# Kernel tuning notes

Measured on AMD Instinct MI355X. Metric: run time of the kernel, lower is better.

## Reference

```python
import jax, jax.numpy as jnp
import numpy as np

MAX_EDGE_LENGTH = 100.0  # filtration cap from cfg['self_supervised']['max_edge_length']


def pairwise_dist(x):
    # Euclidean pairwise distances, [N, N]
    sq = jnp.sum(x * x, axis=-1)
    d2 = sq[:, None] + sq[None, :] - 2.0 * (x @ x.T)
    return jnp.sqrt(jnp.maximum(d2, 0.0) + 1e-12)


def mst_edge_weights(D):
    """Prim's MST over dense distance matrix D [N,N]. Returns N-1 edge weights.
    These weights are exactly the H0 death times of the Vietoris-Rips filtration
    (all H0 features are born at 0)."""
    N = D.shape[0]
    dist0 = D[0]                                   # min distance from tree to each node
    in_tree0 = jnp.zeros((N,), bool).at[0].set(True)

    def step(carry, _):
        dist, in_tree = carry
        masked = jnp.where(in_tree, jnp.inf, dist)
        j = jnp.argmin(masked)
        w = masked[j]                              # weight of edge added to MST
        in_tree = in_tree.at[j].set(True)
        dist = jnp.minimum(dist, D[j])
        return (dist, in_tree), w

    _, weights = jax.lax.scan(step, (dist0, in_tree0), None, length=N - 1)
    return weights


def h0_deaths(x):
    # H0 persistence diagram deaths (births are all 0), capped at max_edge_length
    return jnp.minimum(mst_edge_weights(pairwise_dist(x)), MAX_EDGE_LENGTH)


def setup_inputs() -> dict:
    key = jax.random.key(0)
    k1, k2 = jax.random.split(key)
    N, Dm = 4096, 128
    x_1 = jax.random.normal(k1, (N, Dm), dtype=jnp.float32)
    # correlated second view, as in a siamese/self-supervised setting
    x_2 = x_1 + 0.1 * jax.random.normal(k2, (N, Dm), dtype=jnp.float32)
    return {"x_1": x_1, "x_2": x_2, "plot": 0}


def reference(x_1, x_2, plot):
    # MSE representation loss
    representation_loss = jnp.mean((x_1 - x_2) ** 2)
    # H0 persistence diagrams via Vietoris-Rips (MST formulation)
    d1 = jnp.sort(h0_deaths(x_1))
    d2 = jnp.sort(h0_deaths(x_2))
    # Wasserstein-1 distance between the two H0 diagrams (births all 0,
    # equal cardinality => optimal matching is the sorted matching of deaths)
    topological_loss = jnp.sum(jnp.abs(d1 - d2))
    return representation_loss + topological_loss
```

## Files before the change

### kernel.cpp

```cpp
#include <hip/hip_runtime.h>
#include <hip/hip_fp16.h>

#define NPT 4096
#define DM 128
#define ROUNDS 12
#define INF64 0xFFFFFFFFFFFFFFFFull

typedef _Float16 f16x8 __attribute__((ext_vector_type(8)));
typedef _Float16 f16x2 __attribute__((ext_vector_type(2)));
typedef float f32x4 __attribute__((ext_vector_type(4)));

__global__ __launch_bounds__(256) void init_kernel(unsigned* __restrict__ comp,
                                                   unsigned long long* __restrict__ compbest,
                                                   float* __restrict__ w,
                                                   unsigned* __restrict__ cnt,
                                                   float* __restrict__ rep) {
    int i = blockIdx.x * blockDim.x + threadIdx.x;
    comp[i] = (unsigned)(i & (NPT - 1));
    compbest[i] = INF64;
    w[i] = 0.0f;
    if (i < 2) cnt[i] = 0u;
    if (i == 0) rep[0] = 0.0f;
}

__global__ __launch_bounds__(256) void prep_kernel(const float* __restrict__ x1,
                                                   const float* __restrict__ x2,
                                                   _Float16* __restrict__ Xh,
                                                   float* __restrict__ norms) {
    const int wv = threadIdx.x >> 6, ln = threadIdx.x & 63;
    const int row = blockIdx.x * 4 + wv;
    const float* src = (row < NPT) ? (x1 + (size_t)row * DM)
                                   : (x2 + (size_t)(row - NPT) * DM);
    float2 v = *(const float2*)(src + ln * 2);
    _Float16 h0 = (_Float16)v.x, h1 = (_Float16)v.y;
    f16x2 p; p[0] = h0; p[1] = h1;
    *(f16x2*)(Xh + (size_t)row * DM + ln * 2) = p;
    float a = (float)h0, b = (float)h1;
    float s = a * a + b * b;
    #pragma unroll
    for (int off = 32; off > 0; off >>= 1) s += __shfl_down(s, off);
    if (ln == 0) norms[row] = s;
}

__global__ __launch_bounds__(256) void gram_kernel(const _Float16* __restrict__ Xh,
                                                   const float* __restrict__ norms,
                                                   __half* __restrict__ Dall) {
    const int mat = blockIdx.y;
    const _Float16* __restrict__ X = Xh + (size_t)mat * NPT * DM;
    const float* __restrict__ nrm = norms + mat * NPT;
    __half* __restrict__ D = Dall + (size_t)mat * NPT * NPT;

    int idx = blockIdx.x;
    int J = (int)((sqrtf(8.0f * (float)idx + 1.0f) - 1.0f) * 0.5f);
    while ((J + 1) * (J + 2) / 2 <= idx) ++J;
    while (J * (J + 1) / 2 > idx) --J;
    const int I = idx - J * (J + 1) / 2;

    const int t = threadIdx.x;
    const int wv = t >> 6, ln = t & 63;
    const int rowBase = I * 128 + (wv >> 1) * 64;
    const int colBase = J * 128 + (wv & 1) * 64;
    const int lr = ln & 15;
    const int kg = ln >> 4;

    f32x4 acc[4][4];
    #pragma unroll
    for (int m = 0; m < 4; ++m)
        #pragma unroll
        for (int n = 0; n < 4; ++n)
            acc[m][n] = (f32x4){0.f, 0.f, 0.f, 0.f};

    #pragma unroll
    for (int ks = 0; ks < 4; ++ks) {
        const int k0 = ks * 32 + kg * 8;
        f16x8 a[4], b[4];
        #pragma unroll
        for (int m = 0; m < 4; ++m)
            a[m] = *(const f16x8*)(X + (size_t)(rowBase + m * 16 + lr) * DM + k0);
        #pragma unroll
        for (int n = 0; n < 4; ++n)
            b[n] = *(const f16x8*)(X + (size_t)(colBase + n * 16 + lr) * DM + k0);
        #pragma unroll
        for (int m = 0; m < 4; ++m)
            #pragma unroll
            for (int n = 0; n < 4; ++n)
                acc[m][n] = __builtin_amdgcn_mfma_f32_16x16x32_f16(a[m], b[n], acc[m][n], 0, 0, 0);
    }

    float nr[16], nc[4];
    #pragma unroll
    for (int m = 0; m < 4; ++m)
        #pragma unroll
        for (int q = 0; q < 4; ++q)
            nr[m * 4 + q] = nrm[rowBase + m * 16 + kg * 4 + q];
    #pragma unroll
    for (int n = 0; n < 4; ++n) nc[n] = nrm[colBase + n * 16 + lr];

    #pragma unroll
    for (int m = 0; m < 4; ++m) {
        #pragma unroll
        for (int n = 0; n < 4; ++n) {
            #pragma unroll
            for (int q = 0; q < 4; ++q) {
                const int r = rowBase + m * 16 + kg * 4 + q;
                const int c = colBase + n * 16 + lr;
                float d2 = nr[m * 4 + q] + nc[n] - 2.0f * acc[m][n][q];
                float d = sqrtf(fmaxf(d2, 0.0f) + 1e-12f);
                __half hd = __float2half(d);
                D[(size_t)r * NPT + c] = hd;
                if (I != J) D[(size_t)c * NPT + r] = hd;
            }
        }
    }
}

__global__ __launch_bounds__(1024) void boruvka_a(const __half* __restrict__ Dall,
                                                  const unsigned* __restrict__ compAll,
                                                  unsigned long long* __restrict__ compbestAll,
                                                  const unsigned* __restrict__ cnt) {
    const int mat = blockIdx.y;
    if (cnt[mat] >= NPT - 1u) return;
    const __half* __restrict__ D = Dall + (size_t)mat * NPT * NPT;
    const unsigned* __restrict__ comp = compAll + mat * NPT;
    unsigned long long* __restrict__ compbest = compbestAll + mat * NPT;

    __shared__ unsigned short lcomp[NPT];
    const int t = threadIdx.x;
    for (int i = t; i < NPT; i += 1024) lcomp[i] = (unsigned short)comp[i];
    __syncthreads();

    const int wv = t >> 6, ln = t & 63;
    const int node = blockIdx.x * 16 + wv;
    const unsigned ci = lcomp[node];
    const unsigned* __restrict__ row = (const unsigned*)(D + (size_t)node * NPT);

    unsigned best = 0xFFFFFFFFu;
    #pragma unroll
    for (int k = 0; k < 8; ++k) {
        const int jb = k * 512 + ln * 8;
        uint4 dv = *(const uint4*)(row + (jb >> 1));
        uint4 cv = *(const uint4*)&lcomp[jb];
        const unsigned dp[4] = {dv.x, dv.y, dv.z, dv.w};
        const unsigned cp[4] = {cv.x, cv.y, cv.z, cv.w};
        #pragma unroll
        for (int q = 0; q < 4; ++q) {
            int j0 = jb + q * 2;
            unsigned k0 = (dp[q] << 16) | (unsigned)j0;
            unsigned k1 = (dp[q] & 0xFFFF0000u) | (unsigned)(j0 + 1);
            if ((cp[q] & 0xFFFFu) == ci) k0 = 0xFFFFFFFFu;
            if ((cp[q] >> 16) == ci)     k1 = 0xFFFFFFFFu;
            unsigned m = k0 < k1 ? k0 : k1;
            best = best < m ? best : m;
        }
    }
    #pragma unroll
    for (int off = 32; off > 0; off >>= 1) {
        unsigned o = __shfl_down(best, off);
        best = best < o ? best : o;
    }
    if (ln == 0 && best != 0xFFFFFFFFu) {
        unsigned h = best >> 16;
        unsigned j = best & 0xFFFFu;
        unsigned mn = (unsigned)node < j ? (unsigned)node : j;
        unsigned mx = (unsigned)node < j ? j : (unsigned)node;
        unsigned long long key64 = ((unsigned long long)h << 48) |
                                   ((unsigned long long)mn << 32) |
                                   ((unsigned long long)mx << 16) |
                                   (unsigned long long)j;
        atomicMin(&compbest[ci], key64);
    }
}

__global__ __launch_bounds__(1024) void boruvka_cd(unsigned* __restrict__ compAll,
                                                   unsigned long long* __restrict__ compbestAll,
                                                   float* __restrict__ wAll,
                                                   unsigned* __restrict__ cntAll) {
    const int mat = blockIdx.x;
    if (cntAll[mat] >= NPT - 1u) return;
    unsigned* __restrict__ comp = compAll + mat * NPT;
    unsigned long long* __restrict__ compbest = compbestAll + mat * NPT;
    float* __restrict__ w = wAll + mat * NPT;
    unsigned* __restrict__ cnt = cntAll + mat;

    __shared__ unsigned short par[NPT];
    const int t = threadIdx.x;

    for (int c = t; c < NPT; c += 1024) {
        unsigned p = (unsigned)c;
        unsigned long long key = compbest[c];
        if (comp[c] == (unsigned)c && key != INF64) {
            unsigned jout = (unsigned)(key & 0xFFFFull);
            unsigned c2 = comp[jout];
            unsigned long long k2 = compbest[c2];
            bool mutual = (k2 >> 16) == (key >> 16);
            if (!mutual || (unsigned)c < c2) {
                unsigned short hb = (unsigned short)(key >> 48);
                float wv = fminf(__half2float(__ushort_as_half(hb)), 100.0f);
                unsigned slot = atomicAdd(cnt, 1u);
                w[slot] = wv;
            }
            p = (mutual && (unsigned)c < c2) ? (unsigned)c : c2;
        }
        par[c] = (unsigned short)p;
    }
    __syncthreads();

    for (int it = 0; it < 12; ++it) {
        unsigned short np[4];
        #pragma unroll
        for (int q = 0; q < 4; ++q) np[q] = par[par[t + q * 1024]];
        __syncthreads();
        #pragma unroll
        for (int q = 0; q < 4; ++q) par[t + q * 1024] = np[q];
        __syncthreads();
    }

    for (int c = t; c < NPT; c += 1024) {
        comp[c] = par[comp[c]];
        compbest[c] = INF64;
    }
}

__global__ __launch_bounds__(256) void rep_kernel(const float4* __restrict__ x1,
                                                  const float4* __restrict__ x2,
                                                  float* __restrict__ acc) {
    int idx = blockIdx.x * blockDim.x + threadIdx.x;
    int stride = gridDim.x * blockDim.x;
    float s = 0.f;
    for (int i = idx; i < NPT * DM / 4; i += stride) {
        float4 a = x1[i], b = x2[i];
        float d0 = a.x - b.x, d1 = a.y - b.y, d2 = a.z - b.z, d3 = a.w - b.w;
        s += d0 * d0 + d1 * d1 + d2 * d2 + d3 * d3;
    }
    #pragma unroll
    for (int off = 32; off > 0; off >>= 1) s += __shfl_down(s, off);
    __shared__ float partial[4];
    int wv = threadIdx.x >> 6, ln = threadIdx.x & 63;
    if (ln == 0) partial[wv] = s;
    __syncthreads();
    if (threadIdx.x == 0) {
        float tot = partial[0] + partial[1] + partial[2] + partial[3];
        atomicAdd(acc, tot);
    }
}

__global__ __launch_bounds__(1024) void sort_kernel(float* __restrict__ wAll) {
    float* __restrict__ w = wAll + blockIdx.x * NPT;
    __shared__ float s[NPT];
    const int t = threadIdx.x;
    for (int i = t; i < NPT; i += 1024) s[i] = w[i];
    __syncthreads();

    for (int k = 2; k <= NPT; k <<= 1) {
        for (int j = k >> 1; j > 0; j >>= 1) {
            for (int i = t; i < NPT; i += 1024) {
                int ixj = i ^ j;
                if (ixj > i) {
                    bool up = (i & k) == 0;
                    float a = s[i], b = s[ixj];
                    if ((a > b) == up) { s[i] = b; s[ixj] = a; }
                }
            }
            __syncthreads();
        }
    }
    for (int i = t; i < NPT; i += 1024) w[i] = s[i];
}

__global__ __launch_bounds__(1024) void final2_kernel(const float* __restrict__ w,
                                                      const float* __restrict__ rep,
                                                      float* __restrict__ out) {
    const int t = threadIdx.x;
    float loc = 0.f;
    for (int i = t; i < NPT; i += 1024) loc += fabsf(w[i] - w[NPT + i]);
    #pragma unroll
    for (int off = 32; off > 0; off >>= 1) loc += __shfl_down(loc, off);
    __shared__ float reds[16];
    int wv = t >> 6, ln = t & 63;
    if (ln == 0) reds[wv] = loc;
    __syncthreads();
    if (t == 0) {
        float tot = 0.f;
        #pragma unroll
        for (int i = 0; i < 16; ++i) tot += reds[i];
        out[0] = tot + rep[0] * (1.0f / (NPT * DM));
    }
}

extern "C" void kernel_launch(void* const* d_in, const int* in_sizes, int n_in,
                              void* d_out, int out_size, void* d_ws, size_t ws_size,
                              hipStream_t stream) {
    const float* x1 = (const float*)d_in[0];
    const float* x2 = (const float*)d_in[1];
    float* out = (float*)d_out;

    char* ws = (char*)d_ws;
    __half* D = (__half*)ws;
    size_t off = (size_t)2 * NPT * NPT * sizeof(__half);
    _Float16* Xh = (_Float16*)(ws + off);
    off += (size_t)2 * NPT * DM * sizeof(_Float16);
    float* norms = (float*)(ws + off);
    off += (size_t)2 * NPT * sizeof(float);
    unsigned long long* compbest = (unsigned long long*)(ws + off);
    off += (size_t)2 * NPT * sizeof(unsigned long long);
    float* w = (float*)(ws + off);
    off += (size_t)2 * NPT * sizeof(float);
    unsigned* comp = (unsigned*)(ws + off);
    off += (size_t)2 * NPT * sizeof(unsigned);
    unsigned* cnt = (unsigned*)(ws + off);
    off += 4 * sizeof(unsigned);
    float* rep = (float*)(ws + off);

    init_kernel<<<2 * NPT / 256, 256, 0, stream>>>(comp, compbest, w, cnt, rep);

    prep_kernel<<<2 * NPT / 4, 256, 0, stream>>>(x1, x2, Xh, norms);

    gram_kernel<<<dim3(528, 2), 256, 0, stream>>>(Xh, norms, D);

    for (int r = 0; r < ROUNDS; ++r) {
        boruvka_a<<<dim3(NPT / 16, 2), 1024, 0, stream>>>(D, comp, compbest, cnt);
        boruvka_cd<<<2, 1024, 0, stream>>>(comp, compbest, w, cnt);
    }

    rep_kernel<<<256, 256, 0, stream>>>((const float4*)x1, (const float4*)x2, rep);

    sort_kernel<<<2, 1024, 0, stream>>>(w);

    final2_kernel<<<1, 1024, 0, stream>>>(w, rep, out);
}
```

Before: 341.4 us.

## Fuse Boruvka rounds, sort, and reductions into one cooperative persistent kernel

Replaces the 24 per-round Boruvka kernel launches plus the rep, sort and final kernels with a single cooperative kernel of 256 blocks that uses grid.sync between phases. Rounds exit early once both MSTs are complete. The repr-loss reduction now runs on idle blocks alongside the sort. The gram kernel also drops the symmetric triangular tiling and computes the full square grid, doubling its tiles in exchange for contiguous single writes and no index decoding. The cost is grid-wide barriers and only 256 blocks doing the row-min scans.

```diff
diff --git a/kernel.cpp b/kernel.cpp
--- a/kernel.cpp
+++ b/kernel.cpp
@@ -1,5 +1,8 @@
 #include <hip/hip_runtime.h>
 #include <hip/hip_fp16.h>
+#include <hip/hip_cooperative_groups.h>
+
+namespace cg = cooperative_groups;
 
 #define NPT 4096
 #define DM 128
@@ -50,11 +53,8 @@
     const float* __restrict__ nrm = norms + mat * NPT;
     __half* __restrict__ D = Dall + (size_t)mat * NPT * NPT;
 
-    int idx = blockIdx.x;
-    int J = (int)((sqrtf(8.0f * (float)idx + 1.0f) - 1.0f) * 0.5f);
-    while ((J + 1) * (J + 2) / 2 <= idx) ++J;
-    while (J * (J + 1) / 2 > idx) --J;
-    const int I = idx - J * (J + 1) / 2;
+    const int I = blockIdx.x >> 5;
+    const int J = blockIdx.x & 31;
 
     const int t = threadIdx.x;
     const int wv = t >> 6, ln = t & 63;
@@ -106,184 +106,186 @@
                 const int c = colBase + n * 16 + lr;
                 float d2 = nr[m * 4 + q] + nc[n] - 2.0f * acc[m][n][q];
                 float d = sqrtf(fmaxf(d2, 0.0f) + 1e-12f);
-                __half hd = __float2half(d);
-                D[(size_t)r * NPT + c] = hd;
-                if (I != J) D[(size_t)c * NPT + r] = hd;
-            }
-        }
-    }
-}
-
-__global__ __launch_bounds__(1024) void boruvka_a(const __half* __restrict__ Dall,
-                                                  const unsigned* __restrict__ compAll,
-                                                  unsigned long long* __restrict__ compbestAll,
-                                                  const unsigned* __restrict__ cnt) {
-    const int mat = blockIdx.y;
-    if (cnt[mat] >= NPT - 1u) return;
+                D[(size_t)r * NPT + c] = __float2half(d);
+            }
+        }
+    }
+}
+
+__global__ __launch_bounds__(1024) void mst_coop(const __half* __restrict__ Dall,
+                                                 unsigned* __restrict__ compAll,
+                                                 unsigned long long* __restrict__ compbestAll,
+                                                 float* __restrict__ wAll,
+                                                 unsigned* __restrict__ cntAll,
+                                                 const float4* __restrict__ x1,
+                                                 const float4* __restrict__ x2,
+                                                 float* __restrict__ rep,
+                                                 float* __restrict__ out) {
+    cg::grid_group grid = cg::this_grid();
+    const int bid = blockIdx.x;
+    const int mat = bid >> 7;
+    const int mb = bid & 127;
     const __half* __restrict__ D = Dall + (size_t)mat * NPT * NPT;
-    const unsigned* __restrict__ comp = compAll + mat * NPT;
-    unsigned long long* __restrict__ compbest = compbestAll + mat * NPT;
-
-    __shared__ unsigned short lcomp[NPT];
-    const int t = threadIdx.x;
-    for (int i = t; i < NPT; i += 1024) lcomp[i] = (unsigned short)comp[i];
-    __syncthreads();
-
-    const int wv = t >> 6, ln = t & 63;
-    const int node = blockIdx.x * 16 + wv;
-    const unsigned ci = lcomp[node];
-    const unsigned* __restrict__ row = (const unsigned*)(D + (size_t)node * NPT);
-
-    unsigned best = 0xFFFFFFFFu;
-    #pragma unroll
-    for (int k = 0; k < 8; ++k) {
-        const int jb = k * 512 + ln * 8;
-        uint4 dv = *(const uint4*)(row + (jb >> 1));
-        uint4 cv = *(const uint4*)&lcomp[jb];
-        const unsigned dp[4] = {dv.x, dv.y, dv.z, dv.w};
-        const unsigned cp[4] = {cv.x, cv.y, cv.z, cv.w};
-        #pragma unroll
-        for (int q = 0; q < 4; ++q) {
-            int j0 = jb + q * 2;
-            unsigned k0 = (dp[q] << 16) | (unsigned)j0;
-            unsigned k1 = (dp[q] & 0xFFFF0000u) | (unsigned)(j0 + 1);
-            if ((cp[q] & 0xFFFFu) == ci) k0 = 0xFFFFFFFFu;
-            if ((cp[q] >> 16) == ci)     k1 = 0xFFFFFFFFu;
-            unsigned m = k0 < k1 ? k0 : k1;
-            best = best < m ? best : m;
-        }
-    }
-    #pragma unroll
-    for (int off = 32; off > 0; off >>= 1) {
-        unsigned o = __shfl_down(best, off);
-        best = best < o ? best : o;
-    }
-    if (ln == 0 && best != 0xFFFFFFFFu) {
-        unsigned h = best >> 16;
-        unsigned j = best & 0xFFFFu;
-        unsigned mn = (unsigned)node < j ? (unsigned)node : j;
-        unsigned mx = (unsigned)node < j ? j : (unsigned)node;
-        unsigned long long key64 = ((unsigned long long)h << 48) |
-                                   ((unsigned long long)mn << 32) |
-                                   ((unsigned long long)mx << 16) |
-                                   (unsigned long long)j;
-        atomicMin(&compbest[ci], key64);
-    }
-}
-
-__global__ __launch_bounds__(1024) void boruvka_cd(unsigned* __restrict__ compAll,
-                                                   unsigned long long* __restrict__ compbestAll,
-                                                   float* __restrict__ wAll,
-                                                   unsigned* __restrict__ cntAll) {
-    const int mat = blockIdx.x;
-    if (cntAll[mat] >= NPT - 1u) return;
     unsigned* __restrict__ comp = compAll + mat * NPT;
     unsigned long long* __restrict__ compbest = compbestAll + mat * NPT;
     float* __restrict__ w = wAll + mat * NPT;
     unsigned* __restrict__ cnt = cntAll + mat;
-
-    __shared__ unsigned short par[NPT];
-    const int t = threadIdx.x;
-
-    for (int c = t; c < NPT; c += 1024) {
-        unsigned p = (unsigned)c;
-        unsigned long long key = compbest[c];
-        if (comp[c] == (unsigned)c && key != INF64) {
-            unsigned jout = (unsigned)(key & 0xFFFFull);
-            unsigned c2 = comp[jout];
-            unsigned long long k2 = compbest[c2];
-            bool mutual = (k2 >> 16) == (key >> 16);
-            if (!mutual || (unsigned)c < c2) {
-                unsigned short hb = (unsigned short)(key >> 48);
-                float wv = fminf(__half2float(__ushort_as_half(hb)), 100.0f);
-                unsigned slot = atomicAdd(cnt, 1u);
-                w[slot] = wv;
-            }
-            p = (mutual && (unsigned)c < c2) ? (unsigned)c : c2;
-        }
-        par[c] = (unsigned short)p;
-    }
-    __syncthreads();
-
-    for (int it = 0; it < 12; ++it) {
-        unsigned short np[4];
-        #pragma unroll
-        for (int q = 0; q < 4; ++q) np[q] = par[par[t + q * 1024]];
+    volatile unsigned* vcnt = cntAll;
+
+    __shared__ unsigned short sh16[NPT];
+    __shared__ float shf[NPT];
+    __shared__ float partial[16];
+
+    const int t = threadIdx.x, wv = t >> 6, ln = t & 63;
+
+    for (int r = 0; r < ROUNDS; ++r) {
+        const unsigned c0 = vcnt[0], c1 = vcnt[1];
+        if (c0 >= NPT - 1u && c1 >= NPT - 1u) break;
+        const bool active = ((mat == 0 ? c0 : c1) < NPT - 1u);
+
+        if (active) {
+            for (int i = t; i < NPT; i += 1024) sh16[i] = (unsigned short)comp[i];
+            __syncthreads();
+
+            #pragma unroll
+            for (int rr = 0; rr < 2; ++rr) {
+                const int node = mb * 32 + wv * 2 + rr;
+                const unsigned ci = sh16[node];
+                const unsigned* __restrict__ row = (const unsigned*)(D + (size_t)node * NPT);
+
+                unsigned best = 0xFFFFFFFFu;
+                #pragma unroll
+                for (int k = 0; k < 8; ++k) {
+                    const int jb = k * 512 + ln * 8;
+                    uint4 dv = *(const uint4*)(row + (jb >> 1));
+                    uint4 cv = *(const uint4*)&sh16[jb];
+                    const unsigned dp[4] = {dv.x, dv.y, dv.z, dv.w};
+                    const unsigned cp[4] = {cv.x, cv.y, cv.z, cv.w};
+                    #pragma unroll
+                    for (int q = 0; q < 4; ++q) {
+                        int j0 = jb + q * 2;
+                        unsigned k0 = (dp[q] << 16) | (unsigned)j0;
+                        unsigned k1 = (dp[q] & 0xFFFF0000u) | (unsigned)(j0 + 1);
+                        if ((cp[q] & 0xFFFFu) == ci) k0 = 0xFFFFFFFFu;
+                        if ((cp[q] >> 16) == ci)     k1 = 0xFFFFFFFFu;
+                        unsigned m = k0 < k1 ? k0 : k1;
+                        best = best < m ? best : m;
+                    }
+                }
+                #pragma unroll
+                for (int off = 32; off > 0; off >>= 1) {
+                    unsigned o = __shfl_down(best, off);
+                    best = best < o ? best : o;
+                }
+                if (ln == 0 && best != 0xFFFFFFFFu) {
+                    unsigned h = best >> 16;
+                    unsigned j = best & 0xFFFFu;
+                    unsigned mn = (unsigned)node < j ? (unsigned)node : j;
+                    unsigned mx = (unsigned)node < j ? j : (unsigned)node;
+                    unsigned long long key64 = ((unsigned long long)h << 48) |
+                                               ((unsigned long long)mn << 32) |
+                                               ((unsigned long long)mx << 16) |
+                                               (unsigned long long)j;
+                    atomicMin(&compbest[ci], key64);
+                }
+            }
+        }
+        grid.sync();
+
+        if (active && mb == 0) {
+            for (int c = t; c < NPT; c += 1024) {
+                unsigned p = (unsigned)c;
+                unsigned long long key = compbest[c];
+                if (comp[c] == (unsigned)c && key != INF64) {
+                    unsigned jout = (unsigned)(key & 0xFFFFull);
+                    unsigned c2 = comp[jout];
+                    unsigned long long k2 = compbest[c2];
+                    bool mutual = (k2 >> 16) == (key >> 16);
+                    if (!mutual || (unsigned)c < c2) {
+                        unsigned short hb = (unsigned short)(key >> 48);
+                        float wvv = fminf(__half2float(__ushort_as_half(hb)), 100.0f);
+                        unsigned slot = atomicAdd(cnt, 1u);
+                        w[slot] = wvv;
+                    }
+                    p = (mutual && (unsigned)c < c2) ? (unsigned)c : c2;
+                }
+                sh16[c] = (unsigned short)p;
+            }
+            __syncthreads();
+
+            for (int it = 0; it < 12; ++it) {
+                unsigned short np[4];
+                #pragma unroll
+                for (int q = 0; q < 4; ++q) np[q] = sh16[sh16[t + q * 1024]];
+                __syncthreads();
+                #pragma unroll
+                for (int q = 0; q < 4; ++q) sh16[t + q * 1024] = np[q];
+                __syncthreads();
+            }
+
+            for (int c = t; c < NPT; c += 1024) {
+                comp[c] = sh16[comp[c]];
+                compbest[c] = INF64;
+            }
+        }
+        grid.sync();
+    }
+
+    if (mb == 0) {
+        for (int i = t; i < NPT; i += 1024) shf[i] = w[i];
         __syncthreads();
-        #pragma unroll
-        for (int q = 0; q < 4; ++q) par[t + q * 1024] = np[q];
+        for (int k = 2; k <= NPT; k <<= 1) {
+            for (int j = k >> 1; j > 0; j >>= 1) {
+                for (int i = t; i < NPT; i += 1024) {
+                    int ixj = i ^ j;
+                    if (ixj > i) {
+                        bool up = (i & k) == 0;
+                        float a = shf[i], b = shf[ixj];
+                        if ((a > b) == up) { shf[i] = b; shf[ixj] = a; }
+                    }
+                }
+                __syncthreads();
+            }
+        }
+        for (int i = t; i < NPT; i += 1024) w[i] = shf[i];
+    } else {
+        const int p = mat * 127 + (mb - 1);
+        const int P = 254;
+        float s = 0.f;
+        const int tot4 = NPT * DM / 4;
+        for (int i = p * 1024 + t; i < tot4; i += P * 1024) {
+            float4 a = x1[i], b = x2[i];
+            float d0 = a.x - b.x, d1 = a.y - b.y, d2 = a.z - b.z, d3 = a.w - b.w;
+            s += d0 * d0 + d1 * d1 + d2 * d2 + d3 * d3;
+        }
+        #pragma unroll
+        for (int off = 32; off > 0; off >>= 1) s += __shfl_down(s, off);
+        if (ln == 0) partial[wv] = s;
         __syncthreads();
-    }
-
-    for (int c = t; c < NPT; c += 1024) {
-        comp[c] = par[comp[c]];
-        compbest[c] = INF64;
-    }
-}
-
-__global__ __launch_bounds__(256) void rep_kernel(const float4* __restrict__ x1,
-                                                  const float4* __restrict__ x2,
-                                                  float* __restrict__ acc) {
-    int idx = blockIdx.x * blockDim.x + threadIdx.x;
-    int stride = gridDim.x * blockDim.x;
-    float s = 0.f;
-    for (int i = idx; i < NPT * DM / 4; i += stride) {
-        float4 a = x1[i], b = x2[i];
-        float d0 = a.x - b.x, d1 = a.y - b.y, d2 = a.z - b.z, d3 = a.w - b.w;
-        s += d0 * d0 + d1 * d1 + d2 * d2 + d3 * d3;
-    }
-    #pragma unroll
-    for (int off = 32; off > 0; off >>= 1) s += __shfl_down(s, off);
-    __shared__ float partial[4];
-    int wv = threadIdx.x >> 6, ln = threadIdx.x & 63;
-    if (ln == 0) partial[wv] = s;
-    __syncthreads();
-    if (threadIdx.x == 0) {
-        float tot = partial[0] + partial[1] + partial[2] + partial[3];
-        atomicAdd(acc, tot);
-    }
-}
-
-__global__ __launch_bounds__(1024) void sort_kernel(float* __restrict__ wAll) {
-    float* __restrict__ w = wAll + blockIdx.x * NPT;
-    __shared__ float s[NPT];
-    const int t = threadIdx.x;
-    for (int i = t; i < NPT; i += 1024) s[i] = w[i];
-    __syncthreads();
-
-    for (int k = 2; k <= NPT; k <<= 1) {
-        for (int j = k >> 1; j > 0; j >>= 1) {
-            for (int i = t; i < NPT; i += 1024) {
-                int ixj = i ^ j;
-                if (ixj > i) {
-                    bool up = (i & k) == 0;
-                    float a = s[i], b = s[ixj];
-                    if ((a > b) == up) { s[i] = b; s[ixj] = a; }
-                }
-            }
-            __syncthreads();
-        }
-    }
-    for (int i = t; i < NPT; i += 1024) w[i] = s[i];
-}
-
-__global__ __launch_bounds__(1024) void final2_kernel(const float* __restrict__ w,
-                                                      const float* __restrict__ rep,
-                                                      float* __restrict__ out) {
-    const int t = threadIdx.x;
-    float loc = 0.f;
-    for (int i = t; i < NPT; i += 1024) loc += fabsf(w[i] - w[NPT + i]);
-    #pragma unroll
-    for (int off = 32; off > 0; off >>= 1) loc += __shfl_down(loc, off);
-    __shared__ float reds[16];
-    int wv = t >> 6, ln = t & 63;
-    if (ln == 0) reds[wv] = loc;
-    __syncthreads();
-    if (t == 0) {
-        float tot = 0.f;
-        #pragma unroll
-        for (int i = 0; i < 16; ++i) tot += reds[i];
-        out[0] = tot + rep[0] * (1.0f / (NPT * DM));
+        if (t == 0) {
+            float tb = 0.f;
+            #pragma unroll
+            for (int i = 0; i < 16; ++i) tb += partial[i];
+            atomicAdd(rep, tb);
+        }
+    }
+    grid.sync();
+
+    if (bid == 0) {
+        const float* __restrict__ w0 = wAll;
+        const float* __restrict__ w1 = wAll + NPT;
+        float loc = 0.f;
+        for (int i = t; i < NPT; i += 1024) loc += fabsf(w0[i] - w1[i]);
+        #pragma unroll
+        for (int off = 32; off > 0; off >>= 1) loc += __shfl_down(loc, off);
+        if (ln == 0) partial[wv] = loc;
+        __syncthreads();
+        if (t == 0) {
+            float tot = 0.f;
+            #pragma unroll
+            for (int i = 0; i < 16; ++i) tot += partial[i];
+            out[0] = tot + rep[0] * (1.0f / (NPT * DM));
+        }
     }
 }
 
@@ -315,16 +317,11 @@
 
     prep_kernel<<<2 * NPT / 4, 256, 0, stream>>>(x1, x2, Xh, norms);
 
-    gram_kernel<<<dim3(528, 2), 256, 0, stream>>>(Xh, norms, D);
-
-    for (int r = 0; r < ROUNDS; ++r) {
-        boruvka_a<<<dim3(NPT / 16, 2), 1024, 0, stream>>>(D, comp, compbest, cnt);
-        boruvka_cd<<<2, 1024, 0, stream>>>(comp, compbest, w, cnt);
-    }
-
-    rep_kernel<<<256, 256, 0, stream>>>((const float4*)x1, (const float4*)x2, rep);
-
-    sort_kernel<<<2, 1024, 0, stream>>>(w);
-
-    final2_kernel<<<1, 1024, 0, stream>>>(w, rep, out);
-}
+    gram_kernel<<<dim3(1024, 2), 256, 0, stream>>>(Xh, norms, D);
+
+    const float4* x1f = (const float4*)x1;
+    const float4* x2f = (const float4*)x2;
+    void* args[] = {(void*)&D, (void*)&comp, (void*)&compbest, (void*)&w, (void*)&cnt,
+                    (void*)&x1f, (void*)&x2f, (void*)&rep, (void*)&out};
+    hipLaunchCooperativeKernel((const void*)mst_coop, dim3(256), dim3(1024), args, 0u, stream);
+}
```

New measurement: 518.4 us. 1.52x slower.

## Fuse Boruvka passes via last-block pattern and stage gram tile writes through LDS

Applied to the files above, without the earlier changes.

Merges the per-round Boruvka min-edge search and the contraction step into one kernel: the last block to finish, detected with a per-round atomic counter, performs the component merge and pointer jumping. This halves the number of launches per round. The gram kernel now computes the full 32x32 tile grid instead of only the upper triangle. It stages each tile in shared memory and writes coalesced 16-byte rows, which avoids the scattered transposed stores. The price is twice the MFMA work on the gram and a serial tail in the last block, which relies on threadfence/atomic ordering for correctness.

```diff
diff --git a/kernel.cpp b/kernel.cpp
--- a/kernel.cpp
+++ b/kernel.cpp
@@ -14,12 +14,14 @@
                                                    unsigned long long* __restrict__ compbest,
                                                    float* __restrict__ w,
                                                    unsigned* __restrict__ cnt,
+                                                   unsigned* __restrict__ done,
                                                    float* __restrict__ rep) {
     int i = blockIdx.x * blockDim.x + threadIdx.x;
     comp[i] = (unsigned)(i & (NPT - 1));
     compbest[i] = INF64;
     w[i] = 0.0f;
     if (i < 2) cnt[i] = 0u;
+    if (i < 2 * ROUNDS) done[i] = 0u;
     if (i == 0) rep[0] = 0.0f;
 }
 
@@ -50,16 +52,17 @@
     const float* __restrict__ nrm = norms + mat * NPT;
     __half* __restrict__ D = Dall + (size_t)mat * NPT * NPT;
 
-    int idx = blockIdx.x;
-    int J = (int)((sqrtf(8.0f * (float)idx + 1.0f) - 1.0f) * 0.5f);
-    while ((J + 1) * (J + 2) / 2 <= idx) ++J;
-    while (J * (J + 1) / 2 > idx) --J;
-    const int I = idx - J * (J + 1) / 2;
+    const int I = blockIdx.x >> 5;
+    const int J = blockIdx.x & 31;
+
+    __shared__ _Float16 tile[128 * 136];
 
     const int t = threadIdx.x;
     const int wv = t >> 6, ln = t & 63;
-    const int rowBase = I * 128 + (wv >> 1) * 64;
-    const int colBase = J * 128 + (wv & 1) * 64;
+    const int rloc = (wv >> 1) * 64;
+    const int cloc = (wv & 1) * 64;
+    const int rowBase = I * 128 + rloc;
+    const int colBase = J * 128 + cloc;
     const int lr = ln & 15;
     const int kg = ln >> 4;
 
@@ -102,36 +105,51 @@
         for (int n = 0; n < 4; ++n) {
             #pragma unroll
             for (int q = 0; q < 4; ++q) {
-                const int r = rowBase + m * 16 + kg * 4 + q;
-                const int c = colBase + n * 16 + lr;
+                const int rl = rloc + m * 16 + kg * 4 + q;
+                const int cl = cloc + n * 16 + lr;
                 float d2 = nr[m * 4 + q] + nc[n] - 2.0f * acc[m][n][q];
                 float d = sqrtf(fmaxf(d2, 0.0f) + 1e-12f);
-                __half hd = __float2half(d);
-                D[(size_t)r * NPT + c] = hd;
-                if (I != J) D[(size_t)c * NPT + r] = hd;
+                tile[rl * 136 + cl] = (_Float16)d;
             }
         }
     }
-}
-
-__global__ __launch_bounds__(1024) void boruvka_a(const __half* __restrict__ Dall,
-                                                  const unsigned* __restrict__ compAll,
-                                                  unsigned long long* __restrict__ compbestAll,
-                                                  const unsigned* __restrict__ cnt) {
+    __syncthreads();
+
+    const int tileRow0 = I * 128;
+    #pragma unroll
+    for (int it = 0; it < 8; ++it) {
+        int idx = it * 256 + t;
+        int row = idx >> 4;
+        int ch = idx & 15;
+        *(uint4*)(&D[(size_t)(tileRow0 + row) * NPT + J * 128 + ch * 8]) =
+            *(const uint4*)(&tile[row * 136 + ch * 8]);
+    }
+}
+
+__global__ __launch_bounds__(1024) void boruvka_round(const __half* __restrict__ Dall,
+                                                      unsigned* __restrict__ compAll,
+                                                      unsigned long long* __restrict__ compbestAll,
+                                                      float* __restrict__ wAll,
+                                                      unsigned* __restrict__ cntAll,
+                                                      unsigned* __restrict__ doneAll,
+                                                      int r) {
     const int mat = blockIdx.y;
-    if (cnt[mat] >= NPT - 1u) return;
+    if (cntAll[mat] >= NPT - 1u) return;
     const __half* __restrict__ D = Dall + (size_t)mat * NPT * NPT;
-    const unsigned* __restrict__ comp = compAll + mat * NPT;
+    unsigned* __restrict__ comp = compAll + mat * NPT;
     unsigned long long* __restrict__ compbest = compbestAll + mat * NPT;
-
-    __shared__ unsigned short lcomp[NPT];
-    const int t = threadIdx.x;
-    for (int i = t; i < NPT; i += 1024) lcomp[i] = (unsigned short)comp[i];
-    __syncthreads();
-
-    const int wv = t >> 6, ln = t & 63;
+    float* __restrict__ w = wAll + mat * NPT;
+    unsigned* __restrict__ cnt = cntAll + mat;
+
+    __shared__ unsigned short sh16[NPT];
+    __shared__ int lastFlag;
+    const int t = threadIdx.x, wv = t >> 6, ln = t & 63;
+
+    for (int i = t; i < NPT; i += 1024) sh16[i] = (unsigned short)comp[i];
+    __syncthreads();
+
     const int node = blockIdx.x * 16 + wv;
-    const unsigned ci = lcomp[node];
+    const unsigned ci = sh16[node];
     const unsigned* __restrict__ row = (const unsigned*)(D + (size_t)node * NPT);
 
     unsigned best = 0xFFFFFFFFu;
@@ -139,7 +157,7 @@
     for (int k = 0; k < 8; ++k) {
         const int jb = k * 512 + ln * 8;
         uint4 dv = *(const uint4*)(row + (jb >> 1));
-        uint4 cv = *(const uint4*)&lcomp[jb];
+        uint4 cv = *(const uint4*)&sh16[jb];
         const unsigned dp[4] = {dv.x, dv.y, dv.z, dv.w};
         const unsigned cp[4] = {cv.x, cv.y, cv.z, cv.w};
         #pragma unroll
@@ -169,54 +187,47 @@
                                    (unsigned long long)j;
         atomicMin(&compbest[ci], key64);
     }
-}
-
-__global__ __launch_bounds__(1024) void boruvka_cd(unsigned* __restrict__ compAll,
-                                                   unsigned long long* __restrict__ compbestAll,
-                                                   float* __restrict__ wAll,
-                                                   unsigned* __restrict__ cntAll) {
-    const int mat = blockIdx.x;
-    if (cntAll[mat] >= NPT - 1u) return;
-    unsigned* __restrict__ comp = compAll + mat * NPT;
-    unsigned long long* __restrict__ compbest = compbestAll + mat * NPT;
-    float* __restrict__ w = wAll + mat * NPT;
-    unsigned* __restrict__ cnt = cntAll + mat;
-
-    __shared__ unsigned short par[NPT];
-    const int t = threadIdx.x;
+
+    __threadfence();
+    if (t == 0)
+        lastFlag = (atomicAdd(&doneAll[r * 2 + mat], 1u) == 255u) ? 1 : 0;
+    __syncthreads();
+    if (!lastFlag) return;
 
     for (int c = t; c < NPT; c += 1024) {
         unsigned p = (unsigned)c;
-        unsigned long long key = compbest[c];
-        if (comp[c] == (unsigned)c && key != INF64) {
-            unsigned jout = (unsigned)(key & 0xFFFFull);
-            unsigned c2 = comp[jout];
-            unsigned long long k2 = compbest[c2];
-            bool mutual = (k2 >> 16) == (key >> 16);
-            if (!mutual || (unsigned)c < c2) {
-                unsigned short hb = (unsigned short)(key >> 48);
-                float wv = fminf(__half2float(__ushort_as_half(hb)), 100.0f);
-                unsigned slot = atomicAdd(cnt, 1u);
-                w[slot] = wv;
+        if (comp[c] == (unsigned)c) {
+            unsigned long long key = atomicMin(&compbest[c], INF64);
+            if (key != INF64) {
+                unsigned jout = (unsigned)(key & 0xFFFFull);
+                unsigned c2 = comp[jout];
+                unsigned long long k2 = atomicMin(&compbest[c2], INF64);
+                bool mutual = (k2 >> 16) == (key >> 16);
+                if (!mutual || (unsigned)c < c2) {
+                    unsigned short hb = (unsigned short)(key >> 48);
+                    float wvv = fminf(__half2float(__ushort_as_half(hb)), 100.0f);
+                    unsigned slot = atomicAdd(cnt, 1u);
+                    w[slot] = wvv;
+                }
+                p = (mutual && (unsigned)c < c2) ? (unsigned)c : c2;
             }
-            p = (mutual && (unsigned)c < c2) ? (unsigned)c : c2;
         }
-        par[c] = (unsigned short)p;
+        sh16[c] = (unsigned short)p;
     }
     __syncthreads();
 
     for (int it = 0; it < 12; ++it) {
         unsigned short np[4];
         #pragma unroll
-        for (int q = 0; q < 4; ++q) np[q] = par[par[t + q * 1024]];
+        for (int q = 0; q < 4; ++q) np[q] = sh16[sh16[t + q * 1024]];
         __syncthreads();
         #pragma unroll
-        for (int q = 0; q < 4; ++q) par[t + q * 1024] = np[q];
+        for (int q = 0; q < 4; ++q) sh16[t + q * 1024] = np[q];
         __syncthreads();
     }
 
     for (int c = t; c < NPT; c += 1024) {
-        comp[c] = par[comp[c]];
+        comp[c] = sh16[comp[c]];
         compbest[c] = INF64;
     }
 }
@@ -308,19 +319,19 @@
     unsigned* comp = (unsigned*)(ws + off);
     off += (size_t)2 * NPT * sizeof(unsigned);
     unsigned* cnt = (unsigned*)(ws + off);
-    off += 4 * sizeof(unsigned);
+    off += 2 * sizeof(unsigned);
+    unsigned* done = (unsigned*)(ws + off);
+    off += 2 * ROUNDS * sizeof(unsigned);
     float* rep = (float*)(ws + off);
 
-    init_kernel<<<2 * NPT / 256, 256, 0, stream>>>(comp, compbest, w, cnt, rep);
+    init_kernel<<<2 * NPT / 256, 256, 0, stream>>>(comp, compbest, w, cnt, done, rep);
 
     prep_kernel<<<2 * NPT / 4, 256, 0, stream>>>(x1, x2, Xh, norms);
 
-    gram_kernel<<<dim3(528, 2), 256, 0, stream>>>(Xh, norms, D);
-
-    for (int r = 0; r < ROUNDS; ++r) {
-        boruvka_a<<<dim3(NPT / 16, 2), 1024, 0, stream>>>(D, comp, compbest, cnt);
-        boruvka_cd<<<2, 1024, 0, stream>>>(comp, compbest, w, cnt);
-    }
+    gram_kernel<<<dim3(1024, 2), 256, 0, stream>>>(Xh, norms, D);
+
+    for (int r = 0; r < ROUNDS; ++r)
+        boruvka_round<<<dim3(256, 2), 1024, 0, stream>>>(D, comp, compbest, w, cnt, done, r);
 
     rep_kernel<<<256, 256, 0, stream>>>((const float4*)x1, (const float4*)x2, rep);
 
```

New measurement: 923.8 us. 171% more time.

## Compute full Gram tile grid and stage distance tiles through LDS for coalesced stores

Applied to the files above, without the earlier changes.

The Gram kernel no longer computes only upper-triangular 128x128 tiles and scatters each value to both (r,c) and the transposed (c,r) positions. It now launches all 32x32 tiles, writes results into a padded shared-memory tile, and stores it to global memory with 16-byte vectorized row-contiguous writes. This removes the strided, uncoalesced 2-byte transpose stores at the cost of roughly doubling the MFMA and sqrt work.

```diff
diff --git a/kernel.cpp b/kernel.cpp
--- a/kernel.cpp
+++ b/kernel.cpp
@@ -50,16 +50,17 @@
     const float* __restrict__ nrm = norms + mat * NPT;
     __half* __restrict__ D = Dall + (size_t)mat * NPT * NPT;
 
-    int idx = blockIdx.x;
-    int J = (int)((sqrtf(8.0f * (float)idx + 1.0f) - 1.0f) * 0.5f);
-    while ((J + 1) * (J + 2) / 2 <= idx) ++J;
-    while (J * (J + 1) / 2 > idx) --J;
-    const int I = idx - J * (J + 1) / 2;
+    const int I = blockIdx.x >> 5;
+    const int J = blockIdx.x & 31;
+
+    __shared__ _Float16 tile[128 * 136];
 
     const int t = threadIdx.x;
     const int wv = t >> 6, ln = t & 63;
-    const int rowBase = I * 128 + (wv >> 1) * 64;
-    const int colBase = J * 128 + (wv & 1) * 64;
+    const int rloc = (wv >> 1) * 64;
+    const int cloc = (wv & 1) * 64;
+    const int rowBase = I * 128 + rloc;
+    const int colBase = J * 128 + cloc;
     const int lr = ln & 15;
     const int kg = ln >> 4;
 
@@ -102,15 +103,24 @@
         for (int n = 0; n < 4; ++n) {
             #pragma unroll
             for (int q = 0; q < 4; ++q) {
-                const int r = rowBase + m * 16 + kg * 4 + q;
-                const int c = colBase + n * 16 + lr;
+                const int rl = rloc + m * 16 + kg * 4 + q;
+                const int cl = cloc + n * 16 + lr;
                 float d2 = nr[m * 4 + q] + nc[n] - 2.0f * acc[m][n][q];
                 float d = sqrtf(fmaxf(d2, 0.0f) + 1e-12f);
-                __half hd = __float2half(d);
-                D[(size_t)r * NPT + c] = hd;
-                if (I != J) D[(size_t)c * NPT + r] = hd;
+                tile[rl * 136 + cl] = (_Float16)d;
             }
         }
+    }
+    __syncthreads();
+
+    const int tileRow0 = I * 128;
+    #pragma unroll
+    for (int it = 0; it < 8; ++it) {
+        int idx = it * 256 + t;
+        int row = idx >> 4;
+        int ch = idx & 15;
+        *(uint4*)(&D[(size_t)(tileRow0 + row) * NPT + J * 128 + ch * 8]) =
+            *(const uint4*)(&tile[row * 136 + ch * 8]);
     }
 }
 
@@ -315,7 +325,7 @@
 
     prep_kernel<<<2 * NPT / 4, 256, 0, stream>>>(x1, x2, Xh, norms);
 
-    gram_kernel<<<dim3(528, 2), 256, 0, stream>>>(Xh, norms, D);
+    gram_kernel<<<dim3(1024, 2), 256, 0, stream>>>(Xh, norms, D);
 
     for (int r = 0; r < ROUNDS; ++r) {
         boruvka_a<<<dim3(NPT / 16, 2), 1024, 0, stream>>>(D, comp, compbest, cnt);
```

After: 340.5 us. No clear change (-0.3%).
